# Kernel tuning notes

Measured on AMD Instinct MI355X. Metric: run time of the kernel, lower is better.

Reference implementation:

```python
import jax, jax.numpy as jnp
import numpy as np

B, S, H, D, AD = 64, 200, 4, 256, 256  # batch, max_len, heads, hidden, attribute hidden
HD = D // H  # head dim 64
LN_EPS = 1e-12

PARAM_SHAPES = [
    ('Wq', (D, D)), ('bq', (D,)), ('Wk', (D, D)), ('bk', (D,)), ('Wv', (D, D)), ('bv', (D,)),
    ('Wqp', (D, D)), ('bqp', (D,)), ('Wkp', (D, D)), ('bkp', (D,)),
    ('Waq', (AD, AD)), ('baq', (AD,)), ('Wak', (AD, AD)), ('bak', (AD,)), ('Wav', (AD, AD)), ('bav', (AD,)),
    ('Wqic', (D, AD)), ('bqic', (AD,)), ('Wqci', (AD, D)), ('bqci', (D,)),
    ('Wqpc', (D, AD)), ('bqpc', (AD,)), ('Wqcp', (AD, D)), ('bqcp', (D,)),
    ('Wf1', (S, S)), ('bf1', (S,)), ('Wf2', (S, 1)), ('bf2', (1,)),
    ('Wd', (D, D)), ('bd', (D,)), ('ln_g', (D,)), ('ln_b', (D,)),
    ('Wda', (AD, AD)), ('bda', (AD,)), ('lna_g', (AD,)), ('lna_b', (AD,)),
]


def setup_inputs() -> dict:
    key = jax.random.key(0)
    ks = jax.random.split(key, 8 + len(PARAM_SHAPES))
    inp = {
        'input_tensor': jax.random.normal(ks[0], (B, S, D), jnp.float32),
        'attribute_table': jax.random.normal(ks[1], (1, B, S, 1, AD), jnp.float32),
        'position_embedding': jax.random.normal(ks[2], (B, S, D), jnp.float32),
        'hidden_state_attr': jax.random.normal(ks[3], (1, B, S, 1, AD), jnp.float32),
        'attention_mask': jnp.zeros((B, 1, S, S), jnp.float32),
        'fusion_w': jax.random.uniform(ks[4], (9,), jnp.float32),
        'fusion_wc': jax.random.uniform(ks[5], (4,), jnp.float32),
    }
    for j, (name, shp) in enumerate(PARAM_SHAPES):
        if name.startswith('ln') or name == 'lna_g':
            inp[name] = jnp.ones(shp, jnp.float32) if name.endswith('_g') else jnp.zeros(shp, jnp.float32)
        else:
            inp[name] = jax.random.normal(ks[8 + j], shp, jnp.float32) * 0.02
    return inp


def _forward(input_tensor, attribute_table, position_embedding, hidden_state_attr,
             attention_mask, fusion_w, fusion_wc,
             Wq, bq, Wk, bk, Wv, bv, Wqp, bqp, Wkp, bkp,
             Waq, baq, Wak, bak, Wav, bav, Wqic, bqic, Wqci, bqci,
             Wqpc, bqpc, Wqcp, bqcp, Wf1, bf1, Wf2, bf2,
             Wd, bd, ln_g, ln_b, Wda, bda, lna_g, lna_b):
    lin = lambda x, W, b: x @ W + b

    def heads(x):  # [B,S,D] -> [B,H,S,hd]
        b_, s_, _ = x.shape
        return x.reshape(b_, s_, H, -1).transpose(0, 2, 1, 3)

    def ln(x, g, b):
        m = x.mean(-1, keepdims=True)
        v = ((x - m) ** 2).mean(-1, keepdims=True)
        return (x - m) / jnp.sqrt(v + LN_EPS) * g + b

    attr = attribute_table[0, :, :, 0, :]      # [B,S,AD] (squeeze(-2), feat 0)
    hattr = hidden_state_attr[0, :, :, 0, :]   # [B,S,AD]

    iq, ik, iv = heads(lin(input_tensor, Wq, bq)), heads(lin(input_tensor, Wk, bk)), heads(lin(input_tensor, Wv, bv))
    pq, pk = heads(lin(position_embedding, Wqp, bqp)), heads(lin(position_embedding, Wkp, bkp))
    aq, ak = heads(lin(attr, Waq, baq)), heads(lin(attr, Wak, bak))
    haq, hak, hav = heads(lin(hattr, Waq, baq)), heads(lin(hattr, Wak, bak)), heads(lin(hattr, Wav, bav))
    iqc = heads(lin(input_tensor, Wqic, bqic))
    ciq = heads(lin(attr, Wqci, bqci))
    cqp = heads(lin(attr, Wqcp, bqcp))
    cqp_a = heads(lin(hattr, Wqcp, bqcp))
    pqc = heads(lin(position_embedding, Wqpc, bqpc))

    sc = lambda q, k: jnp.einsum('bhid,bhjd->bhij', q, k)
    pp = sc(pq, pk)
    # 9 item-side streams: ii, ic, ip, ci, cc, cp, pi, pc, pp (matches torch append order)
    raw = jnp.stack([sc(iq, ik), sc(iqc, ak), sc(iq, pk), sc(ciq, ik), sc(aq, ak),
                     sc(cqp, pk), sc(pq, ik), sc(pqc, ak), pp], axis=1)   # [B,9,H,S,S]
    raw_c = jnp.stack([sc(haq, hak), sc(cqp_a, pk), sc(pqc, hak), pp], axis=1)  # [B,4,H,S,S]

    def gate(x, fw):  # VanillaAttention(max_len, max_len) over stream axis
        x = jnp.transpose(x, (0, 2, 3, 1, 4)) * fw[:, None]  # [B,H,S,C,S]
        e = (jax.nn.relu(x @ Wf1 + bf1) @ Wf2 + bf2)[..., 0]  # [B,H,S,C]
        w = jax.nn.softmax(e, axis=-1)
        return jnp.einsum('bhscj,bhsc->bhsj', x, w)  # [B,H,S,S]

    scale = 1.0 / np.sqrt(HD)

    def attend(a, v):
        p = jax.nn.softmax(a * scale + attention_mask, axis=-1)
        ctx = jnp.einsum('bhij,bhjd->bhid', p, v)
        b_ = ctx.shape[0]
        return ctx.transpose(0, 2, 1, 3).reshape(b_, S, -1)

    ctx = attend(gate(raw, fusion_w), iv)
    ctx_c = attend(gate(raw_c, fusion_wc), hav)
    hidden_states = ln(ctx @ Wd + bd + input_tensor, ln_g, ln_b)
    hidden_states_attr = ln(ctx_c @ Wda + bda + hattr, lna_g, lna_b)
    return hidden_states, hidden_states_attr


def reference(input_tensor, attribute_table, position_embedding, hidden_state_attr,
              attention_mask, fusion_w, fusion_wc,
              Wq, bq, Wk, bk, Wv, bv, Wqp, bqp, Wkp, bkp,
              Waq, baq, Wak, bak, Wav, bav, Wqic, bqic, Wqci, bqci,
              Wqpc, bqpc, Wqcp, bqcp, Wf1, bf1, Wf2, bf2,
              Wd, bd, ln_g, ln_b, Wda, bda, lna_g, lna_b):
    return _forward(input_tensor, attribute_table, position_embedding, hidden_state_attr,
                    attention_mask, fusion_w, fusion_wc,
                    Wq, bq, Wk, bk, Wv, bv, Wqp, bqp, Wkp, bkp,
                    Waq, baq, Wak, bak, Wav, bav, Wqic, bqic, Wqci, bqci,
                    Wqpc, bqpc, Wqcp, bqcp, Wf1, bf1, Wf2, bf2,
                    Wd, bd, ln_g, ln_b, Wda, bda, lna_g, lna_b)
```

## Files before the change

### kernel.cpp

```cpp
#include <hip/hip_runtime.h>
#include <cstddef>

typedef __attribute__((ext_vector_type(8))) short bf16x8;
typedef __attribute__((ext_vector_type(4))) short bf16x4;
typedef __attribute__((ext_vector_type(4))) float f32x4;

constexpr int Bc = 64;
constexpr int Sc = 200;
constexpr int Hc = 4;
constexpr int Dc = 256;
constexpr int HDc = 64;
constexpr int NPc = Bc * Sc;
constexpr int NPROJ = 15;
constexpr int NWT   = 17;
constexpr int SLD   = 232;
constexpr float SCALE = 0.125f;


__constant__ int c_KP9[3]  = {1,6,4};
__constant__ int c_QP9[9]  = {0,11,3, 10,5,14, 0,12,3};
__constant__ int c_CG9[9]  = {0,3,6, 1,4,7, 2,5,8};
__constant__ int c_M2S9[9] = {0,24,48,8,32,56,16,40,64};
__constant__ int c_KP4[2]  = {8,4};
__constant__ int c_QP4[4]  = {7,14, 13,3};
__constant__ int c_CG4[4]  = {0,2, 1,3};
__constant__ int c_M2S4[4] = {0,16,8,24};

__device__ __forceinline__ short f2bf(float x) {
    union { float f; unsigned u; } v; v.f = x;
    unsigned r = v.u + 0x7FFFu + ((v.u >> 16) & 1u);
    return (short)(r >> 16);
}
__device__ __forceinline__ float bf2f(short x) {
    union { unsigned u; float f; } v; v.u = ((unsigned)(unsigned short)x) << 16;
    return v.f;
}
__device__ __forceinline__ unsigned cvtpk(float lo, float hi) {
    unsigned r;
    asm("v_cvt_pk_bf16_f32 %0, %1, %2" : "=v"(r) : "v"(lo), "v"(hi));
    return r;
}
__device__ __forceinline__ f32x4 mfma16(bf16x8 a, bf16x8 b, f32x4 c) {
    return __builtin_amdgcn_mfma_f32_16x16x32_bf16(a, b, c, 0, 0, 0);
}

struct ProjArgsM {
    const short* A[NPROJ];
    const float* bias[NPROJ];
};
struct WList { const float* w[NWT]; };

__global__ void cast_in(const float* __restrict__ s0, const float* __restrict__ s1,
                        const float* __restrict__ s2, const float* __restrict__ s3,
                        short* __restrict__ dst) {
    const float* srcs[4] = {s0, s1, s2, s3};
    const float* src = srcs[blockIdx.y];
    short* d = dst + (size_t)blockIdx.y * NPc * Dc;
    int t = blockIdx.x * 256 + threadIdx.x;
    float4 v = ((const float4*)src)[t];
    unsigned p01 = cvtpk(v.x, v.y), p23 = cvtpk(v.z, v.w);
    uint2 st; st.x = p01; st.y = p23;
    *(uint2*)(d + (size_t)t * 4) = st;
}

__global__ void cast_wt(WList wl, short* __restrict__ dst) {
    __shared__ float tbuf[64][65];
    const int p = blockIdx.y;
    const int k0 = (blockIdx.x >> 2) * 64, n0 = (blockIdx.x & 3) * 64;
    const float* W = wl.w[p];
    short* d = dst + (size_t)p * Dc * Dc;
    const int tid = threadIdx.x;
    for (int i = tid; i < 64 * 64; i += 256) {
        int k = i >> 6, n = i & 63;
        tbuf[k][n] = W[(size_t)(k0 + k) * Dc + n0 + n];
    }
    __syncthreads();
    for (int i = tid; i < 64 * 64; i += 256) {
        int n = i >> 6, k = i & 63;
        d[(size_t)(n0 + n) * Dc + k0 + k] = f2bf(tbuf[k][n]);
    }
}

__global__ void wf1t_kernel(const float* __restrict__ Wf1, short* __restrict__ WT) {
    int t = blockIdx.x * 256 + threadIdx.x;
    if (t < 224 * 224) {
        int j = t / 224, i = t % 224;
        WT[t] = (i < Sc && j < Sc) ? f2bf(Wf1[(size_t)i * Sc + j]) : (short)0;
    }
}

__global__ __launch_bounds__(256) void vt_kernel(const short* __restrict__ proj_bf,
                                                 short* __restrict__ vt) {
    const int bid = blockIdx.x;
    const int t  = bid >> 8;
    const int bh = bid & 255;
    const int b = bh >> 2, h = bh & 3;
    const int p = t ? 9 : 2;
    const short* src = proj_bf + ((size_t)p * NPc + (size_t)b * Sc) * Dc + h * HDc;
    short* dst = vt + ((size_t)t * 256 + bh) * 64 * 224;
    __shared__ short tile[200][72];
    const int tid = threadIdx.x;
    for (int idx = tid; idx < 200 * 8; idx += 256) {
        int j = idx >> 3, c8 = idx & 7;
        *(bf16x8*)(&tile[j][c8 * 8]) = *(const bf16x8*)(src + (size_t)j * Dc + c8 * 8);
    }
    __syncthreads();
    for (int idx = tid; idx < 64 * 28; idx += 256) {
        int d = idx / 28, c8 = idx % 28;
        bf16x8 o;
        #pragma unroll
        for (int i = 0; i < 8; ++i) {
            int j = c8 * 8 + i;
            o[i] = (j < 200) ? tile[j][d] : (short)0;
        }
        *(bf16x8*)(dst + (size_t)d * 224 + c8 * 8) = o;
    }
}

__global__ __launch_bounds__(256, 4) void proj_mfma(
    ProjArgsM args, const short* __restrict__ WTall, short* __restrict__ proj_bf)
{
    const int p  = blockIdx.y;
    const int m0 = blockIdx.x * 64;
    const short* __restrict__ A   = args.A[p];
    const short* __restrict__ WTp = WTall + (size_t)p * Dc * Dc;
    const float* __restrict__ bias = args.bias[p];
    short* __restrict__ ob = proj_bf + (size_t)p * NPc * Dc;

    __shared__ __align__(16) short As[64 * 264];
    const int tid = threadIdx.x;
    const int lane = tid & 63, w = tid >> 6;
    const int l15 = lane & 15, l4 = lane >> 4;

    for (int t = tid; t < 64 * 32; t += 256) {
        int r = t >> 5, c8 = t & 31;
        *(bf16x8*)(As + r * 264 + c8 * 8) = *(const bf16x8*)(A + (size_t)(m0 + r) * Dc + c8 * 8);
    }
    __syncthreads();

    f32x4 acc[4][4];
    #pragma unroll
    for (int mi = 0; mi < 4; ++mi)
        #pragma unroll
        for (int ni = 0; ni < 4; ++ni) acc[mi][ni] = (f32x4){};

    const int nb = w * 64;
    #pragma unroll
    for (int ks = 0; ks < 8; ++ks) {
        bf16x8 bfr[4];
        #pragma unroll
        for (int ni = 0; ni < 4; ++ni)
            bfr[ni] = *(const bf16x8*)(WTp + (size_t)(nb + ni * 16 + l15) * Dc + ks * 32 + l4 * 8);
        #pragma unroll
        for (int mi = 0; mi < 4; ++mi) {
            bf16x8 a = *(const bf16x8*)(As + (mi * 16 + l15) * 264 + ks * 32 + l4 * 8);
            #pragma unroll
            for (int ni = 0; ni < 4; ++ni)
                acc[mi][ni] = mfma16(a, bfr[ni], acc[mi][ni]);
        }
    }

    float bv[4];
    #pragma unroll
    for (int ni = 0; ni < 4; ++ni) bv[ni] = bias[nb + ni * 16 + l15];
    #pragma unroll
    for (int mi = 0; mi < 4; ++mi) {
        #pragma unroll
        for (int ni = 0; ni < 4; ++ni) {
            int n = nb + ni * 16 + l15;
            int m = m0 + mi * 16 + l4 * 4;
            unsigned p01 = cvtpk(acc[mi][ni][0] + bv[ni], acc[mi][ni][1] + bv[ni]);
            unsigned p23 = cvtpk(acc[mi][ni][2] + bv[ni], acc[mi][ni][3] + bv[ni]);
            ob[(size_t)(m + 0) * Dc + n] = (short)p01;
            ob[(size_t)(m + 1) * Dc + n] = (short)(p01 >> 16);
            ob[(size_t)(m + 2) * Dc + n] = (short)p23;
            ob[(size_t)(m + 3) * Dc + n] = (short)(p23 >> 16);
        }
    }
}

template <int CH, int NG, int CPG, int QT, int MT2>
__device__ void fused_body(
    int bid,
    const short* __restrict__ proj_bf,
    const short* __restrict__ vtb,
    const float* __restrict__ fw,
    const float* __restrict__ mask,
    const short* __restrict__ WT,
    const float* __restrict__ bf1,
    const float* __restrict__ Wf2,
    short* __restrict__ ctx_out,
    const int* KP, const int* QP, const int* CG, const int* M2S,
    short* Sl, float* fwl, float* bf1l, float* wf2l)
{
    constexpr int GR    = CPG * 8;
    constexpr int VROWS = NG * GR;
    constexpr int SROWS = MT2 * 16;
    constexpr int NW    = 4;

    const int tid = threadIdx.x;
    const int rt  = bid % 25;
    const int h   = (bid / 25) & 3;
    const int b   = bid / 100;
    const int r0  = rt * 8;
    const int lane = tid & 63, wv = tid >> 6;
    const int l15 = lane & 15, l4 = lane >> 4;
    const int brow0 = b * Sc + r0;

    {
        bf16x8 z = {};
        if constexpr (SROWS > VROWS) {
            for (int t = tid; t < (SROWS - VROWS) * 28; t += 256) {
                int r = VROWS + t / 28, c8 = t % 28;
                *(bf16x8*)(Sl + r * SLD + c8 * 8) = z;
            }
        }
        for (int t = tid; t < VROWS * 3; t += 256) {
            int r = t / 3, c8 = t % 3;
            *(bf16x8*)(Sl + r * SLD + 200 + c8 * 8) = z;
        }
    }
    if (tid < 224) {
        bf1l[tid] = (tid < Sc) ? bf1[tid] : 0.f;
        wf2l[tid] = (tid < Sc) ? Wf2[tid] : 0.f;
    }
    if (tid < CH) fwl[tid] = fw[tid];

    bf16x8 af[NG][QT][2];
    #pragma unroll
    for (int g = 0; g < NG; ++g) {
        #pragma unroll
        for (int t = 0; t < QT; ++t) {
            int sr = t * 16 + l15;
            int kk = (sr < GR) ? (sr >> 3) : 0;
            int rr = (sr < GR) ? (sr & 7) : 0;
            const short* qp = proj_bf + ((size_t)QP[g * CPG + kk] * NPc + brow0 + rr) * Dc + h * HDc;
            #pragma unroll
            for (int ks = 0; ks < 2; ++ks)
                af[g][t][ks] = *(const bf16x8*)(qp + ks * 32 + l4 * 8);
        }
    }
    __syncthreads();

    {
        const short* Kb[NG];
        #pragma unroll
        for (int g = 0; g < NG; ++g)
            Kb[g] = proj_bf + ((size_t)KP[g] * NPc + (size_t)b * Sc) * Dc + h * HDc;

        float fwv[NG][QT];
        #pragma unroll
        for (int g = 0; g < NG; ++g)
            #pragma unroll
            for (int t = 0; t < QT; ++t) {
                int k = t * 2 + (l4 >> 1);
                fwv[g][t] = (k < CPG) ? fwl[CG[g * CPG + k]] : 0.f;
            }

        bf16x8 cur[NG][2];
        int nt = wv;
        {
            int j = nt * 16 + l15;
            #pragma unroll
            for (int g = 0; g < NG; ++g) {
                cur[g][0] = *(const bf16x8*)(Kb[g] + (size_t)j * Dc + l4 * 8);
                cur[g][1] = *(const bf16x8*)(Kb[g] + (size_t)j * Dc + 32 + l4 * 8);
            }
        }
        while (nt < 13) {
            const int ntn = nt + NW;
            bf16x8 nxt[NG][2];
            if (ntn < 13) {
                int j2 = ntn * 16 + l15;
                #pragma unroll
                for (int g = 0; g < NG; ++g) {
                    nxt[g][0] = *(const bf16x8*)(Kb[g] + (size_t)j2 * Dc + l4 * 8);
                    nxt[g][1] = *(const bf16x8*)(Kb[g] + (size_t)j2 * Dc + 32 + l4 * 8);
                }
            }
            const int j = nt * 16 + l15;
            const bool jv = (j < Sc);
            #pragma unroll
            for (int g = 0; g < NG; ++g) {
                #pragma unroll
                for (int t = 0; t < QT; ++t) {
                    f32x4 c = {};
                    c = mfma16(af[g][t][0], cur[g][0], c);
                    c = mfma16(af[g][t][1], cur[g][1], c);
                    int k = t * 2 + (l4 >> 1);
                    if (jv && k < CPG) {
                        int srb = g * GR + t * 16 + l4 * 4;
                        float f = fwv[g][t];
                        unsigned p01 = cvtpk(c[0] * f, c[1] * f);
                        unsigned p23 = cvtpk(c[2] * f, c[3] * f);
                        Sl[(srb + 0) * SLD + j] = (short)p01;
                        Sl[(srb + 1) * SLD + j] = (short)(p01 >> 16);
                        Sl[(srb + 2) * SLD + j] = (short)p23;
                        Sl[(srb + 3) * SLD + j] = (short)(p23 >> 16);
                    }
                }
            }
            #pragma unroll
            for (int g = 0; g < NG; ++g) { cur[g][0] = nxt[g][0]; cur[g][1] = nxt[g][1]; }
            nt = ntn;
        }
    }
    __syncthreads();

    {
        float epart[MT2];
        #pragma unroll
        for (int mt = 0; mt < MT2; ++mt) epart[mt] = 0.f;

        for (int nt = wv; nt < 13; nt += NW) {
            const int jr = nt * 16 + l15;
            bf16x8 wfrag[7];
            #pragma unroll
            for (int ks = 0; ks < 7; ++ks)
                wfrag[ks] = *(const bf16x8*)(WT + (size_t)jr * 224 + ks * 32 + l4 * 8);
            f32x4 cg[MT2];
            #pragma unroll
            for (int mt = 0; mt < MT2; ++mt) cg[mt] = (f32x4){};
            #pragma unroll
            for (int ks = 0; ks < 7; ++ks) {
                #pragma unroll
                for (int mt = 0; mt < MT2; ++mt) {
                    bf16x8 bb = *(const bf16x8*)(Sl + (mt * 16 + l15) * SLD + ks * 32 + l4 * 8);
                    cg[mt] = mfma16(wfrag[ks], bb, cg[mt]);
                }
            }
            float4 b1 = *(const float4*)(bf1l + nt * 16 + l4 * 4);
            float4 w2 = *(const float4*)(wf2l + nt * 16 + l4 * 4);
            #pragma unroll
            for (int mt = 0; mt < MT2; ++mt) {
                float s = fmaxf(cg[mt][0] + b1.x, 0.f) * w2.x
                        + fmaxf(cg[mt][1] + b1.y, 0.f) * w2.y
                        + fmaxf(cg[mt][2] + b1.z, 0.f) * w2.z
                        + fmaxf(cg[mt][3] + b1.w, 0.f) * w2.w;
                s += __shfl_xor(s, 16, 64);
                s += __shfl_xor(s, 32, 64);
                epart[mt] += s;
            }
        }
        if (l4 == 0) {
            #pragma unroll
            for (int mt = 0; mt < MT2; ++mt)
                *(float*)(Sl + (size_t)(mt * 16 + l15) * SLD + 224 + wv * 2) = epart[mt];
        }
    }
    __syncthreads();

    const int ra = wv, rb = wv + 4;

    float wchA[CH], wchB[CH];
    {
        float eA[CH], eB[CH];
        float mxA = -1e30f, mxB = -1e30f;
        #pragma unroll
        for (int c = 0; c < CH; ++c) {
            int m = M2S[c];
            float sA = 0.f, sB = 0.f;
            #pragma unroll
            for (int w = 0; w < NW; ++w) {
                sA += *(const float*)(Sl + (size_t)(m + ra) * SLD + 224 + w * 2);
                sB += *(const float*)(Sl + (size_t)(m + rb) * SLD + 224 + w * 2);
            }
            eA[c] = sA; eB[c] = sB;
            mxA = fmaxf(mxA, sA); mxB = fmaxf(mxB, sB);
        }
        float suA = 0.f, suB = 0.f;
        #pragma unroll
        for (int c = 0; c < CH; ++c) {
            eA[c] = __expf(eA[c] - mxA); suA += eA[c];
            eB[c] = __expf(eB[c] - mxB); suB += eB[c];
        }
        float ivA = 1.f / suA, ivB = 1.f / suB;
        #pragma unroll
        for (int c = 0; c < CH; ++c) { wchA[c] = eA[c] * ivA; wchB[c] = eB[c] * ivB; }
    }

    const bool act = lane < 50;
    const int j4 = lane * 4;
    float vA[4], vB[4];
    if (act) {
        const float* mbase = mask + ((size_t)b * Sc + r0) * Sc;
        float aA[4] = {0.f, 0.f, 0.f, 0.f};
        float aB[4] = {0.f, 0.f, 0.f, 0.f};
        #pragma unroll
        for (int c = 0; c < CH; ++c) {
            bf16x4 sA = *(const bf16x4*)(Sl + (size_t)(M2S[c] + ra) * SLD + j4);
            bf16x4 sB = *(const bf16x4*)(Sl + (size_t)(M2S[c] + rb) * SLD + j4);
            float wA = wchA[c], wB = wchB[c];
            #pragma unroll
            for (int i = 0; i < 4; ++i) {
                aA[i] += wA * bf2f(sA[i]);
                aB[i] += wB * bf2f(sB[i]);
            }
        }
        float4 mA = *(const float4*)(mbase + (size_t)ra * Sc + j4);
        float4 mB = *(const float4*)(mbase + (size_t)rb * Sc + j4);
        vA[0] = aA[0] * SCALE + mA.x; vA[1] = aA[1] * SCALE + mA.y;
        vA[2] = aA[2] * SCALE + mA.z; vA[3] = aA[3] * SCALE + mA.w;
        vB[0] = aB[0] * SCALE + mB.x; vB[1] = aB[1] * SCALE + mB.y;
        vB[2] = aB[2] * SCALE + mB.z; vB[3] = aB[3] * SCALE + mB.w;
    } else {
        #pragma unroll
        for (int i = 0; i < 4; ++i) { vA[i] = -1e30f; vB[i] = -1e30f; }
    }

    {
        float mx = fmaxf(fmaxf(vA[0], vA[1]), fmaxf(vA[2], vA[3]));
        #pragma unroll
        for (int off = 32; off >= 1; off >>= 1) mx = fmaxf(mx, __shfl_xor(mx, off, 64));
        float p0 = act ? __expf(vA[0] - mx) : 0.f;
        float p1 = act ? __expf(vA[1] - mx) : 0.f;
        float p2 = act ? __expf(vA[2] - mx) : 0.f;
        float p3 = act ? __expf(vA[3] - mx) : 0.f;
        float s = p0 + p1 + p2 + p3;
        #pragma unroll
        for (int off = 32; off >= 1; off >>= 1) s += __shfl_xor(s, off, 64);
        float inv = 1.f / s;
        if (act) {
            uint2 st;
            st.x = cvtpk(p0 * inv, p1 * inv);
            st.y = cvtpk(p2 * inv, p3 * inv);
            *(uint2*)(Sl + (size_t)ra * SLD + j4) = st;
        }
    }
    {
        float mx = fmaxf(fmaxf(vB[0], vB[1]), fmaxf(vB[2], vB[3]));
        #pragma unroll
        for (int off = 32; off >= 1; off >>= 1) mx = fmaxf(mx, __shfl_xor(mx, off, 64));
        float p0 = act ? __expf(vB[0] - mx) : 0.f;
        float p1 = act ? __expf(vB[1] - mx) : 0.f;
        float p2 = act ? __expf(vB[2] - mx) : 0.f;
        float p3 = act ? __expf(vB[3] - mx) : 0.f;
        float s = p0 + p1 + p2 + p3;
        #pragma unroll
        for (int off = 32; off >= 1; off >>= 1) s += __shfl_xor(s, off, 64);
        float inv = 1.f / s;
        if (act) {
            uint2 st;
            st.x = cvtpk(p0 * inv, p1 * inv);
            st.y = cvtpk(p2 * inv, p3 * inv);
            *(uint2*)(Sl + (size_t)rb * SLD + j4) = st;
        }
    }
    __syncthreads();

    {
        const short* vb = vtb + ((size_t)(b * Hc + h) * 64) * 224;
        const int nb = wv * 16;
        f32x4 c0 = {}, c1 = {};
        #pragma unroll
        for (int ks = 0; ks < 7; ks += 2) {
            bf16x8 aa = *(const bf16x8*)(Sl + l15 * SLD + ks * 32 + l4 * 8);
            bf16x8 bb = *(const bf16x8*)(vb + (size_t)(nb + l15) * 224 + ks * 32 + l4 * 8);
            c0 = mfma16(aa, bb, c0);
            if (ks + 1 < 7) {
                bf16x8 aa1 = *(const bf16x8*)(Sl + l15 * SLD + (ks + 1) * 32 + l4 * 8);
                bf16x8 bb1 = *(const bf16x8*)(vb + (size_t)(nb + l15) * 224 + (ks + 1) * 32 + l4 * 8);
                c1 = mfma16(aa1, bb1, c1);
            }
        }
        if (l4 < 2) {
            #pragma unroll
            for (int i = 0; i < 4; ++i) {
                int row = l4 * 4 + i;
                ctx_out[((size_t)(brow0 + row)) * Dc + h * HDc + nb + l15] =
                    f2bf(c0[i] + c1[i]);
            }
        }
    }
}

__global__ __launch_bounds__(256, 3) void fused9(
    const short* __restrict__ proj_bf,
    const short* __restrict__ vt,
    const float* __restrict__ fw9,
    const float* __restrict__ fw4,
    const float* __restrict__ mask,
    const short* __restrict__ WT,
    const float* __restrict__ bf1,
    const float* __restrict__ Wf2,
    short* __restrict__ ctxb,
    short* __restrict__ ctxcb)
{
    __shared__ __align__(16) short Sl[80 * SLD];
    __shared__ float fwl[9];
    __shared__ float bf1l[224];
    __shared__ float wf2l[224];

    const int d    = blockIdx.x;
    const int xcd  = d & 7;
    const int slot = d >> 3;
    const int chunk = (slot / 25) * 8 + xcd;
    const int pos   = slot % 25;
    const int bid   = chunk * 25 + pos;

    if (bid < 6400) {
        fused_body<9, 3, 3, 2, 5>(bid, proj_bf, vt, fw9, mask, WT, bf1, Wf2, ctxb,
                                  c_KP9, c_QP9, c_CG9, c_M2S9,
                                  Sl, fwl, bf1l, wf2l);
    } else {
        fused_body<4, 2, 2, 1, 2>(bid - 6400, proj_bf, vt + (size_t)256 * 64 * 224,
                                  fw4, mask, WT, bf1, Wf2, ctxcb,
                                  c_KP4, c_QP4, c_CG4, c_M2S4,
                                  Sl, fwl, bf1l, wf2l);
    }
}

__global__ __launch_bounds__(256, 3) void out_ln_mfma(
    const short* __restrict__ Ab,
    const short* __restrict__ WTp,
    const float* __restrict__ bias,
    const float* __restrict__ resid,
    const float* __restrict__ gamma,
    const float* __restrict__ beta,
    float* __restrict__ out)
{
    const int m0 = blockIdx.x * 32;
    __shared__ __align__(16) short As[32 * 264];
    __shared__ float ylds[32][257];
    const int tid = threadIdx.x;
    const int lane = tid & 63, wv = tid >> 6;
    const int l15 = lane & 15, l4 = lane >> 4;

    for (int t = tid; t < 32 * 32; t += 256) {
        int r = t >> 5, c8 = t & 31;
        *(bf16x8*)(As + r * 264 + c8 * 8) = *(const bf16x8*)(Ab + (size_t)(m0 + r) * Dc + c8 * 8);
    }
    __syncthreads();

    const int nb = wv * 64;
    f32x4 acc[2][4];
    #pragma unroll
    for (int mi = 0; mi < 2; ++mi)
        #pragma unroll
        for (int ni = 0; ni < 4; ++ni) acc[mi][ni] = (f32x4){};

    #pragma unroll
    for (int ks = 0; ks < 8; ++ks) {
        bf16x8 bfr[4];
        #pragma unroll
        for (int ni = 0; ni < 4; ++ni)
            bfr[ni] = *(const bf16x8*)(WTp + (size_t)(nb + ni * 16 + l15) * Dc + ks * 32 + l4 * 8);
        #pragma unroll
        for (int mi = 0; mi < 2; ++mi) {
            bf16x8 a = *(const bf16x8*)(As + (mi * 16 + l15) * 264 + ks * 32 + l4 * 8);
            #pragma unroll
            for (int ni = 0; ni < 4; ++ni)
                acc[mi][ni] = mfma16(a, bfr[ni], acc[mi][ni]);
        }
    }

    #pragma unroll
    for (int mi = 0; mi < 2; ++mi) {
        #pragma unroll
        for (int ni = 0; ni < 4; ++ni) {
            int n = nb + ni * 16 + l15;
            float bv = bias[n];
            #pragma unroll
            for (int i = 0; i < 4; ++i) {
                int row = mi * 16 + l4 * 4 + i;
                ylds[row][n] = acc[mi][ni][i] + bv + resid[(size_t)(m0 + row) * Dc + n];
            }
        }
    }
    __syncthreads();

    for (int r = wv * 8; r < wv * 8 + 8; ++r) {
        float v4[4];
        float s = 0.f, s2 = 0.f;
        #pragma unroll
        for (int t4 = 0; t4 < 4; ++t4) {
            float v = ylds[r][t4 * 64 + lane];
            v4[t4] = v;
            s += v; s2 += v * v;
        }
        #pragma unroll
        for (int off = 32; off >= 1; off >>= 1) {
            s  += __shfl_xor(s, off, 64);
            s2 += __shfl_xor(s2, off, 64);
        }
        float m   = s * (1.f / 256.f);
        float var = s2 * (1.f / 256.f) - m * m;
        float rstd = rsqrtf(var + 1e-12f);
        #pragma unroll
        for (int t4 = 0; t4 < 4; ++t4) {
            int ccol = t4 * 64 + lane;
            out[(size_t)(m0 + r) * Dc + ccol] = (v4[t4] - m) * rstd * gamma[ccol] + beta[ccol];
        }
    }
}

extern "C" void kernel_launch(void* const* d_in, const int* in_sizes, int n_in,
                              void* d_out, int out_size, void* d_ws, size_t ws_size,
                              hipStream_t stream) {
    const float* X    = (const float*)d_in[0];
    const float* AT   = (const float*)d_in[1];
    const float* P    = (const float*)d_in[2];
    const float* HA   = (const float*)d_in[3];
    const float* mask = (const float*)d_in[4];
    const float* fw   = (const float*)d_in[5];
    const float* fwc  = (const float*)d_in[6];

    const float* Wq   = (const float*)d_in[7];
    const float* bq   = (const float*)d_in[8];
    const float* Wk   = (const float*)d_in[9];
    const float* bk   = (const float*)d_in[10];
    const float* Wv   = (const float*)d_in[11];
    const float* bv   = (const float*)d_in[12];
    const float* Wqp  = (const float*)d_in[13];
    const float* bqp  = (const float*)d_in[14];
    const float* Wkp  = (const float*)d_in[15];
    const float* bkp  = (const float*)d_in[16];
    const float* Waq  = (const float*)d_in[17];
    const float* baq  = (const float*)d_in[18];
    const float* Wak  = (const float*)d_in[19];
    const float* bak  = (const float*)d_in[20];
    const float* Wav  = (const float*)d_in[21];
    const float* bav  = (const float*)d_in[22];
    const float* Wqic = (const float*)d_in[23];
    const float* bqic = (const float*)d_in[24];
    const float* Wqci = (const float*)d_in[25];
    const float* bqci = (const float*)d_in[26];
    const float* Wqpc = (const float*)d_in[27];
    const float* bqpc = (const float*)d_in[28];
    const float* Wqcp = (const float*)d_in[29];
    const float* bqcp = (const float*)d_in[30];
    const float* Wf1  = (const float*)d_in[31];
    const float* bf1  = (const float*)d_in[32];
    const float* Wf2  = (const float*)d_in[33];
    const float* bf2  = (const float*)d_in[34];
    const float* Wd   = (const float*)d_in[35];
    const float* bd   = (const float*)d_in[36];
    const float* ln_g = (const float*)d_in[37];
    const float* ln_b = (const float*)d_in[38];
    const float* Wda  = (const float*)d_in[39];
    const float* bda  = (const float*)d_in[40];
    const float* lna_g= (const float*)d_in[41];
    const float* lna_b= (const float*)d_in[42];

    char* w = (char*)d_ws;
    short* proj_bf = (short*)w;  w += (size_t)NPROJ * NPc * Dc * sizeof(short);
    short* WTall   = (short*)w;  w += (size_t)NWT * Dc * Dc * sizeof(short);
    short* WTf1    = (short*)w;  w += (size_t)224 * 224 * sizeof(short);
    short* inb     = (short*)w;  w += (size_t)4 * NPc * Dc * sizeof(short);
    short* vt      = (short*)w;  w += (size_t)2 * 256 * 64 * 224 * sizeof(short);
    short* ctxb    = (short*)w;  w += (size_t)NPc * Dc * sizeof(short);
    short* ctxcb   = (short*)w;  w += (size_t)NPc * Dc * sizeof(short);

    const int aid[NPROJ] = {0,0,0,2,2,1,1,3,3,3,0,1,1,3,2};
    const float* Wmat[NWT] = {Wq, Wk, Wv, Wqp, Wkp, Waq, Wak, Waq, Wak, Wav,
                              Wqic, Wqci, Wqcp, Wqcp, Wqpc, Wd, Wda};
    const float* bmat[NPROJ] = {bq, bk, bv, bqp, bkp, baq, bak, baq, bak, bav,
                                bqic, bqci, bqcp, bqcp, bqpc};

    ProjArgsM pm;
    WList wl;
    for (int i = 0; i < NPROJ; i++) {
        pm.A[i]    = inb + (size_t)aid[i] * NPc * Dc;
        pm.bias[i] = bmat[i];
    }
    for (int i = 0; i < NWT; i++) wl.w[i] = Wmat[i];

    cast_in<<<dim3(NPc * Dc / 4 / 256, 4), 256, 0, stream>>>(X, AT, P, HA, inb);
    cast_wt<<<dim3(16, NWT), 256, 0, stream>>>(wl, WTall);
    wf1t_kernel<<<(224 * 224 + 255) / 256, 256, 0, stream>>>(Wf1, WTf1);

    proj_mfma<<<dim3(NPc / 64, NPROJ), 256, 0, stream>>>(pm, WTall, proj_bf);

    vt_kernel<<<512, 256, 0, stream>>>(proj_bf, vt);

    fused9<<<12800, 256, 0, stream>>>(proj_bf, vt, fw, fwc, mask, WTf1, bf1, Wf2, ctxb, ctxcb);

    float* out0 = (float*)d_out;
    float* out1 = out0 + (size_t)NPc * Dc;
    out_ln_mfma<<<NPc / 32, 256, 0, stream>>>(ctxb,  WTall + (size_t)15 * Dc * Dc, bd,
                                              X,  ln_g,  ln_b,  out0);
    out_ln_mfma<<<NPc / 32, 256, 0, stream>>>(ctxcb, WTall + (size_t)16 * Dc * Dc, bda,
                                              HA, lna_g, lna_b, out1);
}
```

Baseline: 473.8 us.

## Merge prep kernels, widen fused attention block to 8 waves, merge output LN launches

```diff
diff --git a/kernel.cpp b/kernel.cpp
--- a/kernel.cpp
+++ b/kernel.cpp
@@ -50,42 +50,49 @@
 };
 struct WList { const float* w[NWT]; };
 
-__global__ void cast_in(const float* __restrict__ s0, const float* __restrict__ s1,
-                        const float* __restrict__ s2, const float* __restrict__ s3,
-                        short* __restrict__ dst) {
-    const float* srcs[4] = {s0, s1, s2, s3};
-    const float* src = srcs[blockIdx.y];
-    short* d = dst + (size_t)blockIdx.y * NPc * Dc;
-    int t = blockIdx.x * 256 + threadIdx.x;
-    float4 v = ((const float4*)src)[t];
-    unsigned p01 = cvtpk(v.x, v.y), p23 = cvtpk(v.z, v.w);
-    uint2 st; st.x = p01; st.y = p23;
-    *(uint2*)(d + (size_t)t * 4) = st;
-}
-
-__global__ void cast_wt(WList wl, short* __restrict__ dst) {
+__global__ __launch_bounds__(256) void prep_kernel(
+    const float* __restrict__ X, const float* __restrict__ AT,
+    const float* __restrict__ P, const float* __restrict__ HA,
+    short* __restrict__ inb,
+    WList wl, short* __restrict__ WTall,
+    const float* __restrict__ Wf1, short* __restrict__ WTf1)
+{
     __shared__ float tbuf[64][65];
-    const int p = blockIdx.y;
-    const int k0 = (blockIdx.x >> 2) * 64, n0 = (blockIdx.x & 3) * 64;
-    const float* W = wl.w[p];
-    short* d = dst + (size_t)p * Dc * Dc;
+    const int bid = blockIdx.x;
     const int tid = threadIdx.x;
-    for (int i = tid; i < 64 * 64; i += 256) {
-        int k = i >> 6, n = i & 63;
-        tbuf[k][n] = W[(size_t)(k0 + k) * Dc + n0 + n];
-    }
-    __syncthreads();
-    for (int i = tid; i < 64 * 64; i += 256) {
-        int n = i >> 6, k = i & 63;
-        d[(size_t)(n0 + n) * Dc + k0 + k] = f2bf(tbuf[k][n]);
-    }
-}
-
-__global__ void wf1t_kernel(const float* __restrict__ Wf1, short* __restrict__ WT) {
-    int t = blockIdx.x * 256 + threadIdx.x;
-    if (t < 224 * 224) {
-        int j = t / 224, i = t % 224;
-        WT[t] = (i < Sc && j < Sc) ? f2bf(Wf1[(size_t)i * Sc + j]) : (short)0;
+
+    if (bid < 12800) {
+        int ten = bid / 3200, blk = bid - ten * 3200;
+        const float* srcs[4] = {X, AT, P, HA};
+        const float* src = srcs[ten];
+        short* d = inb + (size_t)ten * NPc * Dc;
+        int t = blk * 256 + tid;
+        float4 v = ((const float4*)src)[t];
+        uint2 st;
+        st.x = cvtpk(v.x, v.y);
+        st.y = cvtpk(v.z, v.w);
+        *(uint2*)(d + (size_t)t * 4) = st;
+    } else if (bid < 13072) {
+        int q = bid - 12800;
+        int p = q >> 4, tile = q & 15;
+        int k0 = (tile >> 2) * 64, n0 = (tile & 3) * 64;
+        const float* W = wl.w[p];
+        short* d = WTall + (size_t)p * Dc * Dc;
+        for (int i = tid; i < 64 * 64; i += 256) {
+            int k = i >> 6, n = i & 63;
+            tbuf[k][n] = W[(size_t)(k0 + k) * Dc + n0 + n];
+        }
+        __syncthreads();
+        for (int i = tid; i < 64 * 64; i += 256) {
+            int n = i >> 6, k = i & 63;
+            d[(size_t)(n0 + n) * Dc + k0 + k] = f2bf(tbuf[k][n]);
+        }
+    } else {
+        int t = (bid - 13072) * 256 + tid;
+        if (t < 224 * 224) {
+            int j = t / 224, i = t % 224;
+            WTf1[t] = (i < Sc && j < Sc) ? f2bf(Wf1[(size_t)i * Sc + j]) : (short)0;
+        }
     }
 }
 
@@ -191,12 +198,12 @@
     const float* __restrict__ Wf2,
     short* __restrict__ ctx_out,
     const int* KP, const int* QP, const int* CG, const int* M2S,
-    short* Sl, float* fwl, float* bf1l, float* wf2l)
+    short* Sl, float* evw, float* fwl, float* bf1l, float* wf2l)
 {
     constexpr int GR    = CPG * 8;
     constexpr int VROWS = NG * GR;
     constexpr int SROWS = MT2 * 16;
-    constexpr int NW    = 4;
+    constexpr int NW    = 8;
 
     const int tid = threadIdx.x;
     const int rt  = bid % 25;
@@ -210,12 +217,12 @@
     {
         bf16x8 z = {};
         if constexpr (SROWS > VROWS) {
-            for (int t = tid; t < (SROWS - VROWS) * 28; t += 256) {
+            for (int t = tid; t < (SROWS - VROWS) * 28; t += 512) {
                 int r = VROWS + t / 28, c8 = t % 28;
                 *(bf16x8*)(Sl + r * SLD + c8 * 8) = z;
             }
         }
-        for (int t = tid; t < VROWS * 3; t += 256) {
+        for (int t = tid; t < VROWS * 3; t += 512) {
             int r = t / 3, c8 = t % 3;
             *(bf16x8*)(Sl + r * SLD + 200 + c8 * 8) = z;
         }
@@ -307,6 +314,12 @@
     }
     __syncthreads();
 
+    const bool act = lane < 50;
+    const int j4 = lane * 4;
+    float4 mrow = make_float4(0.f, 0.f, 0.f, 0.f);
+    if (act)
+        mrow = *(const float4*)(mask + ((size_t)b * Sc + r0 + wv) * Sc + j4);
+
     {
         float epart[MT2];
         #pragma unroll
@@ -345,67 +358,56 @@
         if (l4 == 0) {
             #pragma unroll
             for (int mt = 0; mt < MT2; ++mt)
-                *(float*)(Sl + (size_t)(mt * 16 + l15) * SLD + 224 + wv * 2) = epart[mt];
-        }
-    }
-    __syncthreads();
-
-    const int ra = wv, rb = wv + 4;
-
-    float wchA[CH], wchB[CH];
+                evw[wv * SROWS + mt * 16 + l15] = epart[mt];
+        }
+    }
+    __syncthreads();
+
+    const int ra = wv;
+
+    const short* vb = vtb + ((size_t)(b * Hc + h) * 64) * 224;
+    const int nb = (wv & 3) * 16;
+    bf16x8 vfr[7];
+    if (wv < 4) {
+        #pragma unroll
+        for (int ks = 0; ks < 7; ++ks)
+            vfr[ks] = *(const bf16x8*)(vb + (size_t)(nb + l15) * 224 + ks * 32 + l4 * 8);
+    }
+
+    float wch[CH];
     {
-        float eA[CH], eB[CH];
-        float mxA = -1e30f, mxB = -1e30f;
+        float e[CH]; float mx = -1e30f;
         #pragma unroll
         for (int c = 0; c < CH; ++c) {
-            int m = M2S[c];
-            float sA = 0.f, sB = 0.f;
-            #pragma unroll
-            for (int w = 0; w < NW; ++w) {
-                sA += *(const float*)(Sl + (size_t)(m + ra) * SLD + 224 + w * 2);
-                sB += *(const float*)(Sl + (size_t)(m + rb) * SLD + 224 + w * 2);
-            }
-            eA[c] = sA; eB[c] = sB;
-            mxA = fmaxf(mxA, sA); mxB = fmaxf(mxB, sB);
-        }
-        float suA = 0.f, suB = 0.f;
-        #pragma unroll
-        for (int c = 0; c < CH; ++c) {
-            eA[c] = __expf(eA[c] - mxA); suA += eA[c];
-            eB[c] = __expf(eB[c] - mxB); suB += eB[c];
-        }
-        float ivA = 1.f / suA, ivB = 1.f / suB;
-        #pragma unroll
-        for (int c = 0; c < CH; ++c) { wchA[c] = eA[c] * ivA; wchB[c] = eB[c] * ivB; }
-    }
-
-    const bool act = lane < 50;
-    const int j4 = lane * 4;
-    float vA[4], vB[4];
+            int m = M2S[c] + ra;
+            float s = 0.f;
+            #pragma unroll
+            for (int w = 0; w < NW; ++w) s += evw[w * SROWS + m];
+            e[c] = s; mx = fmaxf(mx, s);
+        }
+        float su = 0.f;
+        #pragma unroll
+        for (int c = 0; c < CH; ++c) { e[c] = __expf(e[c] - mx); su += e[c]; }
+        float iv = 1.f / su;
+        #pragma unroll
+        for (int c = 0; c < CH; ++c) wch[c] = e[c] * iv;
+    }
+
+    float vA[4];
     if (act) {
-        const float* mbase = mask + ((size_t)b * Sc + r0) * Sc;
         float aA[4] = {0.f, 0.f, 0.f, 0.f};
-        float aB[4] = {0.f, 0.f, 0.f, 0.f};
         #pragma unroll
         for (int c = 0; c < CH; ++c) {
             bf16x4 sA = *(const bf16x4*)(Sl + (size_t)(M2S[c] + ra) * SLD + j4);
-            bf16x4 sB = *(const bf16x4*)(Sl + (size_t)(M2S[c] + rb) * SLD + j4);
-            float wA = wchA[c], wB = wchB[c];
-            #pragma unroll
-            for (int i = 0; i < 4; ++i) {
-                aA[i] += wA * bf2f(sA[i]);
-                aB[i] += wB * bf2f(sB[i]);
-            }
-        }
-        float4 mA = *(const float4*)(mbase + (size_t)ra * Sc + j4);
-        float4 mB = *(const float4*)(mbase + (size_t)rb * Sc + j4);
-        vA[0] = aA[0] * SCALE + mA.x; vA[1] = aA[1] * SCALE + mA.y;
-        vA[2] = aA[2] * SCALE + mA.z; vA[3] = aA[3] * SCALE + mA.w;
-        vB[0] = aB[0] * SCALE + mB.x; vB[1] = aB[1] * SCALE + mB.y;
-        vB[2] = aB[2] * SCALE + mB.z; vB[3] = aB[3] * SCALE + mB.w;
+            float wA = wch[c];
+            #pragma unroll
+            for (int i = 0; i < 4; ++i) aA[i] += wA * bf2f(sA[i]);
+        }
+        vA[0] = aA[0] * SCALE + mrow.x; vA[1] = aA[1] * SCALE + mrow.y;
+        vA[2] = aA[2] * SCALE + mrow.z; vA[3] = aA[3] * SCALE + mrow.w;
     } else {
         #pragma unroll
-        for (int i = 0; i < 4; ++i) { vA[i] = -1e30f; vB[i] = -1e30f; }
+        for (int i = 0; i < 4; ++i) vA[i] = -1e30f;
     }
 
     {
@@ -427,40 +429,17 @@
             *(uint2*)(Sl + (size_t)ra * SLD + j4) = st;
         }
     }
-    {
-        float mx = fmaxf(fmaxf(vB[0], vB[1]), fmaxf(vB[2], vB[3]));
-        #pragma unroll
-        for (int off = 32; off >= 1; off >>= 1) mx = fmaxf(mx, __shfl_xor(mx, off, 64));
-        float p0 = act ? __expf(vB[0] - mx) : 0.f;
-        float p1 = act ? __expf(vB[1] - mx) : 0.f;
-        float p2 = act ? __expf(vB[2] - mx) : 0.f;
-        float p3 = act ? __expf(vB[3] - mx) : 0.f;
-        float s = p0 + p1 + p2 + p3;
-        #pragma unroll
-        for (int off = 32; off >= 1; off >>= 1) s += __shfl_xor(s, off, 64);
-        float inv = 1.f / s;
-        if (act) {
-            uint2 st;
-            st.x = cvtpk(p0 * inv, p1 * inv);
-            st.y = cvtpk(p2 * inv, p3 * inv);
-            *(uint2*)(Sl + (size_t)rb * SLD + j4) = st;
-        }
-    }
-    __syncthreads();
-
-    {
-        const short* vb = vtb + ((size_t)(b * Hc + h) * 64) * 224;
-        const int nb = wv * 16;
+    __syncthreads();
+
+    if (wv < 4) {
         f32x4 c0 = {}, c1 = {};
         #pragma unroll
         for (int ks = 0; ks < 7; ks += 2) {
             bf16x8 aa = *(const bf16x8*)(Sl + l15 * SLD + ks * 32 + l4 * 8);
-            bf16x8 bb = *(const bf16x8*)(vb + (size_t)(nb + l15) * 224 + ks * 32 + l4 * 8);
-            c0 = mfma16(aa, bb, c0);
+            c0 = mfma16(aa, vfr[ks], c0);
             if (ks + 1 < 7) {
                 bf16x8 aa1 = *(const bf16x8*)(Sl + l15 * SLD + (ks + 1) * 32 + l4 * 8);
-                bf16x8 bb1 = *(const bf16x8*)(vb + (size_t)(nb + l15) * 224 + (ks + 1) * 32 + l4 * 8);
-                c1 = mfma16(aa1, bb1, c1);
+                c1 = mfma16(aa1, vfr[ks + 1], c1);
             }
         }
         if (l4 < 2) {
@@ -474,7 +453,7 @@
     }
 }
 
-__global__ __launch_bounds__(256, 3) void fused9(
+__global__ __launch_bounds__(512) void fused10(
     const short* __restrict__ proj_bf,
     const short* __restrict__ vt,
     const float* __restrict__ fw9,
@@ -487,6 +466,7 @@
     short* __restrict__ ctxcb)
 {
     __shared__ __align__(16) short Sl[80 * SLD];
+    __shared__ float evw[8 * 80];
     __shared__ float fwl[9];
     __shared__ float bf1l[224];
     __shared__ float wf2l[224];
@@ -501,25 +481,35 @@
     if (bid < 6400) {
         fused_body<9, 3, 3, 2, 5>(bid, proj_bf, vt, fw9, mask, WT, bf1, Wf2, ctxb,
                                   c_KP9, c_QP9, c_CG9, c_M2S9,
-                                  Sl, fwl, bf1l, wf2l);
+                                  Sl, evw, fwl, bf1l, wf2l);
     } else {
         fused_body<4, 2, 2, 1, 2>(bid - 6400, proj_bf, vt + (size_t)256 * 64 * 224,
                                   fw4, mask, WT, bf1, Wf2, ctxcb,
                                   c_KP4, c_QP4, c_CG4, c_M2S4,
-                                  Sl, fwl, bf1l, wf2l);
-    }
-}
-
-__global__ __launch_bounds__(256, 3) void out_ln_mfma(
-    const short* __restrict__ Ab,
-    const short* __restrict__ WTp,
-    const float* __restrict__ bias,
-    const float* __restrict__ resid,
-    const float* __restrict__ gamma,
-    const float* __restrict__ beta,
-    float* __restrict__ out)
+                                  Sl, evw, fwl, bf1l, wf2l);
+    }
+}
+
+__global__ __launch_bounds__(256, 3) void out_ln2(
+    const short* __restrict__ ctxb, const short* __restrict__ ctxcb,
+    const short* __restrict__ WT15, const short* __restrict__ WT16,
+    const float* __restrict__ bd,   const float* __restrict__ bda,
+    const float* __restrict__ X,    const float* __restrict__ HA,
+    const float* __restrict__ g0,   const float* __restrict__ be0,
+    const float* __restrict__ g1,   const float* __restrict__ be1,
+    float* __restrict__ out0,       float* __restrict__ out1)
 {
-    const int m0 = blockIdx.x * 32;
+    const int bidx = blockIdx.x;
+    const bool sec = bidx >= 400;
+    const short* Ab    = sec ? ctxcb : ctxb;
+    const short* WTp   = sec ? WT16 : WT15;
+    const float* bias  = sec ? bda : bd;
+    const float* resid = sec ? HA : X;
+    const float* gamma = sec ? g1 : g0;
+    const float* beta  = sec ? be1 : be0;
+    float* out = sec ? out1 : out0;
+    const int m0 = (sec ? bidx - 400 : bidx) * 32;
+
     __shared__ __align__(16) short As[32 * 264];
     __shared__ float ylds[32][257];
     const int tid = threadIdx.x;
@@ -665,20 +655,18 @@
     }
     for (int i = 0; i < NWT; i++) wl.w[i] = Wmat[i];
 
-    cast_in<<<dim3(NPc * Dc / 4 / 256, 4), 256, 0, stream>>>(X, AT, P, HA, inb);
-    cast_wt<<<dim3(16, NWT), 256, 0, stream>>>(wl, WTall);
-    wf1t_kernel<<<(224 * 224 + 255) / 256, 256, 0, stream>>>(Wf1, WTf1);
+    prep_kernel<<<13268, 256, 0, stream>>>(X, AT, P, HA, inb, wl, WTall, Wf1, WTf1);
 
     proj_mfma<<<dim3(NPc / 64, NPROJ), 256, 0, stream>>>(pm, WTall, proj_bf);
 
     vt_kernel<<<512, 256, 0, stream>>>(proj_bf, vt);
 
-    fused9<<<12800, 256, 0, stream>>>(proj_bf, vt, fw, fwc, mask, WTf1, bf1, Wf2, ctxb, ctxcb);
-
-    float* out0 = (float*)d_out;
-    float* out1 = out0 + (size_t)NPc * Dc;
-    out_ln_mfma<<<NPc / 32, 256, 0, stream>>>(ctxb,  WTall + (size_t)15 * Dc * Dc, bd,
-                                              X,  ln_g,  ln_b,  out0);
-    out_ln_mfma<<<NPc / 32, 256, 0, stream>>>(ctxcb, WTall + (size_t)16 * Dc * Dc, bda,
-                                              HA, lna_g, lna_b, out1);
-}
+    fused10<<<12800, 512, 0, stream>>>(proj_bf, vt, fw, fwc, mask, WTf1, bf1, Wf2, ctxb, ctxcb);
+
+    out_ln2<<<800, 256, 0, stream>>>(ctxb, ctxcb,
+                                     WTall + (size_t)15 * Dc * Dc,
+                                     WTall + (size_t)16 * Dc * Dc,
+                                     bd, bda, X, HA,
+                                     ln_g, ln_b, lna_g, lna_b,
+                                     (float*)d_out, (float*)d_out + (size_t)NPc * Dc);
+}
```

Result: slower. 589.3 us (+24.4%).
